# Kernel optimization log

Measured on AMD Instinct MI355X. Metric: run time of the kernel, lower is better.

Reference implementation:

```python
import jax, jax.numpy as jnp
import numpy as np

E, H, K = 8, 256, 2        # num_experts, hidden_size, top-k
B, S, TD, ID = 16, 1024, 768, 1024
EPS = 1e-5

def gelu(x):
    return jax.nn.gelu(x, approximate=False)  # torch nn.GELU default = exact erf

def layer_norm(x, g, b):
    m = jnp.mean(x, axis=-1, keepdims=True)
    v = jnp.var(x, axis=-1, keepdims=True)
    return (x - m) * jax.lax.rsqrt(v + EPS) * g + b

def moe(x, gate_W, gate_b, W1, b1, W2, b2):
    # x: [B,S,H]
    gates = jax.nn.softmax(x @ gate_W + gate_b, axis=-1)        # [B,S,E]
    topv, topi = jax.lax.top_k(gates, K)                        # [B,S,K]
    # dense all-expert compute (faithful to the torch loop+stack)
    h = gelu(jnp.einsum('bsh,ehg->bseg', x, W1) + b1)           # [B,S,E,H]
    eo = jnp.einsum('bseg,egh->bseh', h, W2) + b2               # [B,S,E,H]
    sel = jnp.take_along_axis(eo, topi[..., None], axis=2)      # [B,S,K,H]
    return jnp.sum(sel * topv[..., None], axis=2)               # [B,S,H]

def setup_inputs() -> dict:
    key = jax.random.key(0)
    ks = jax.random.split(key, 12)
    def n(k, shape, scale=0.05):
        return jax.random.normal(k, shape, jnp.float32) * scale
    return dict(
        x=jax.random.normal(ks[0], (B, S, TD), jnp.float32),
        We=n(ks[1], (TD, H)), be=jnp.zeros((H,), jnp.float32),
        l2_emb=n(ks[2], (H,)), cl_emb=n(ks[3], (H,)),
        gate_W=n(ks[4], (H, E)), gate_b=jnp.zeros((E,), jnp.float32),
        W1=n(ks[5], (E, H, H)), b1=jnp.zeros((E, H), jnp.float32),
        W2=n(ks[6], (E, H, H)), b2=jnp.zeros((E, H), jnp.float32),
        l2_g=jnp.ones((H,), jnp.float32), l2_b=jnp.zeros((H,), jnp.float32),
        cl_g=jnp.ones((H,), jnp.float32), cl_b=jnp.zeros((H,), jnp.float32),
        Wt2i=n(ks[7], (H, ID)), bt2i=jnp.zeros((ID,), jnp.float32),
        Wcl=n(ks[8], (H, H)), bcl=jnp.zeros((H,), jnp.float32),
    )

def reference(x, We, be, l2_emb, cl_emb, gate_W, gate_b, W1, b1, W2, b2,
              l2_g, l2_b, cl_g, cl_b, Wt2i, bt2i, Wcl, bcl):
    # task == 'text2image'
    x = gelu(x @ We + be)                                       # text_embed + gelu
    l2_in = x + l2_emb
    cl_in = x + cl_emb
    l2 = gelu(layer_norm(moe(l2_in, gate_W, gate_b, W1, b1, W2, b2), l2_g, l2_b)) + l2_in
    cl = gelu(layer_norm(moe(cl_in, gate_W, gate_b, W1, b1, W2, b2), cl_g, cl_b)) + cl_in
    l2_res = l2 @ Wt2i + bt2i                                   # text_to_image head
    cl_res = cl @ Wcl + bcl                                     # cl_text_to_image head
    return (l2_res, cl_res)
```

## Files before the change

### kernel.cpp

```cpp
#include <hip/hip_runtime.h>
#include <hip/hip_bf16.h>
#include <math.h>

typedef __bf16 bf16_t;
typedef __bf16 bf16x4 __attribute__((ext_vector_type(4)));
typedef __bf16 bf16x8 __attribute__((ext_vector_type(8)));
typedef float  f32x4  __attribute__((ext_vector_type(4)));

#define NTOK 16384
#define HD   256
#define TD   768
#define ID   1024
#define NPAIR 32768
#define MOE_TPB 520
#define FLAG_CAP 4096

__device__ inline float fast_erf(float x){
    float ax = fabsf(x);
    float t = 1.0f / (1.0f + 0.3275911f*ax);
    float y = t*(0.254829592f + t*(-0.284496736f + t*(1.421413741f +
              t*(-1.453152027f + t*1.061405429f))));
    float e = 1.0f - y*__expf(-ax*ax);
    return copysignf(e, x);
}
__device__ inline float gelu_f(float x){
    return 0.5f * x * (1.0f + fast_erf(x * 0.70710678118654752f));
}
__device__ inline bf16x4 cvt4(float4 a){
    bf16x4 o; o[0]=(bf16_t)a.x; o[1]=(bf16_t)a.y; o[2]=(bf16_t)a.z; o[3]=(bf16_t)a.w; return o;
}
__device__ inline f32x4 mfma16(bf16x8 a, bf16x8 b, f32x4 c){
    return __builtin_amdgcn_mfma_f32_16x16x32_bf16(a, b, c, 0, 0, 0);
}
__device__ inline void gload_lds16(const void* g, void* l){
    __builtin_amdgcn_global_load_lds(
        (const __attribute__((address_space(1))) unsigned int*)g,
        (__attribute__((address_space(3))) unsigned int*)l, 16, 0, 0);
}

__global__ void k_zero(int* meta){
    if (threadIdx.x < 64) meta[threadIdx.x] = 0;
}

__global__ __launch_bounds__(256) void k_convert(
    const float* __restrict__ We, const float* __restrict__ W1,
    const float* __restrict__ W2, const float* __restrict__ Wt,
    const float* __restrict__ Wc,
    bf16_t* __restrict__ WeHi, bf16_t* __restrict__ WeLo,
    bf16_t* __restrict__ W1T,
    bf16_t* __restrict__ W2T, bf16_t* __restrict__ WtT, bf16_t* __restrict__ WcT)
{
    __shared__ float T[64][65];
    int job = blockIdx.x;
    const float* src; bf16_t* dst; bf16_t* dst2 = nullptr;
    int K, N, k0, n0;
    if (job < 48){ src = We;  dst = WeHi; dst2 = WeLo; K = 768; N = 256;
        k0 = (job>>2)*64; n0 = (job&3)*64;
    } else if (job < 176){ int e = (job-48)>>4, tj = (job-48)&15;
        src = W1 + ((size_t)e<<16); dst = W1T + ((size_t)e<<16); K=256; N=256;
        k0 = (tj>>2)*64; n0 = (tj&3)*64;
    } else if (job < 304){ int e = (job-176)>>4, tj = (job-176)&15;
        src = W2 + ((size_t)e<<16); dst = W2T + ((size_t)e<<16); K=256; N=256;
        k0 = (tj>>2)*64; n0 = (tj&3)*64;
    } else if (job < 368){ int tj = job-304; src = Wt; dst = WtT; K=256; N=1024;
        k0 = (tj>>4)*64; n0 = (tj&15)*64;
    } else { int tj = job-368; src = Wc; dst = WcT; K=256; N=256;
        k0 = (tj>>2)*64; n0 = (tj&3)*64;
    }
    int t = threadIdx.x;
    #pragma unroll
    for (int u=0;u<4;++u){
        int unit = u*256 + t;
        int r = unit>>4, c4 = (unit&15)*4;
        float4 v = *(const float4*)(src + (size_t)(k0+r)*N + n0 + c4);
        T[r][c4] = v.x; T[r][c4+1] = v.y; T[r][c4+2] = v.z; T[r][c4+3] = v.w;
    }
    __syncthreads();
    #pragma unroll
    for (int u=0;u<4;++u){
        int unit = u*256 + t;
        int rn = unit>>4, c4 = (unit&15)*4;
        bf16x4 h, l;
        #pragma unroll
        for (int j=0;j<4;++j){
            float f = T[c4+j][rn];
            bf16_t hb = (bf16_t)f;
            h[j] = hb; l[j] = (bf16_t)(f - (float)hb);
        }
        *(bf16x4*)(dst + (size_t)(n0+rn)*K + k0 + c4) = h;
        if (dst2) *(bf16x4*)(dst2 + (size_t)(n0+rn)*K + k0 + c4) = l;
    }
}

__global__ __launch_bounds__(256) void k_embed(
    const float* __restrict__ x, const bf16_t* __restrict__ WeHi,
    const bf16_t* __restrict__ WeLo,
    const float* __restrict__ be, const float* __restrict__ l2e,
    const float* __restrict__ cle,
    float* __restrict__ l2f, float* __restrict__ clf)
{
    __shared__ bf16_t Ah[128][40];
    __shared__ bf16_t Al[128][40];
    __shared__ bf16_t Bh[64][40];
    __shared__ bf16_t Bl[64][40];
    int row0 = blockIdx.x*128, col0 = blockIdx.y*64;
    int t = threadIdx.x, wave = t>>6, lane = t&63;
    int wm = wave>>1, wn = wave&1;
    f32x4 acc[4][2] = {};
    for (int k0 = 0; k0 < TD; k0 += 32){
        __syncthreads();
        #pragma unroll
        for (int u=0; u<4; ++u){
            int fi = u*256 + t, r = fi>>3, q = fi&7;
            float4 v = *(const float4*)(x + (size_t)(row0+r)*TD + k0 + q*4);
            bf16x4 h = cvt4(v);
            float4 rl;
            rl.x = v.x-(float)h[0]; rl.y = v.y-(float)h[1];
            rl.z = v.z-(float)h[2]; rl.w = v.w-(float)h[3];
            *(bf16x4*)(&Ah[r][q*4]) = h;
            *(bf16x4*)(&Al[r][q*4]) = cvt4(rl);
        }
        {
            int r = t>>2, q = t&3;
            *(bf16x8*)(&Bh[r][q*8]) = *(const bf16x8*)(WeHi + (size_t)(col0+r)*TD + k0 + q*8);
            *(bf16x8*)(&Bl[r][q*8]) = *(const bf16x8*)(WeLo + (size_t)(col0+r)*TD + k0 + q*8);
        }
        __syncthreads();
        int kq = lane>>4, lr = lane&15;
        bf16x8 ah[4], al[4], bh[2], bl[2];
        #pragma unroll
        for (int m=0;m<4;++m){
            ah[m] = *(const bf16x8*)(&Ah[wm*64 + m*16 + lr][kq*8]);
            al[m] = *(const bf16x8*)(&Al[wm*64 + m*16 + lr][kq*8]);
        }
        #pragma unroll
        for (int n=0;n<2;++n){
            bh[n] = *(const bf16x8*)(&Bh[wn*32 + n*16 + lr][kq*8]);
            bl[n] = *(const bf16x8*)(&Bl[wn*32 + n*16 + lr][kq*8]);
        }
        #pragma unroll
        for (int m=0;m<4;++m)
            #pragma unroll
            for (int n=0;n<2;++n){
                acc[m][n] = mfma16(ah[m], bh[n], acc[m][n]);
                acc[m][n] = mfma16(ah[m], bl[n], acc[m][n]);
                acc[m][n] = mfma16(al[m], bh[n], acc[m][n]);
            }
    }
    int kq = lane>>4, lr = lane&15;
    #pragma unroll
    for (int n=0;n<2;++n){
        int col = col0 + wn*32 + n*16 + lr;
        float bv = be[col], lv = l2e[col], cv = cle[col];
        #pragma unroll
        for (int m=0;m<4;++m)
            #pragma unroll
            for (int r=0;r<4;++r){
                int row = row0 + wm*64 + m*16 + kq*4 + r;
                float v = gelu_f(acc[m][n][r] + bv);
                l2f[(size_t)row*HD + col] = v + lv;
                clf[(size_t)row*HD + col] = v + cv;
            }
    }
}

__global__ __launch_bounds__(256) void k_gate(
    const float* __restrict__ l2f, const float* __restrict__ clf,
    const float* __restrict__ gW, const float* __restrict__ gb,
    float* __restrict__ topv, int* __restrict__ topi,
    int* __restrict__ flaglist, int* __restrict__ nflag,
    bf16_t* __restrict__ l2h, bf16_t* __restrict__ clh)
{
    __shared__ float gw[2048];
    int t = threadIdx.x;
    for (int i=t; i<2048; i+=256) gw[i] = gW[i];
    __syncthreads();
    int wave = t>>6, lane = t&63;
    int idx = blockIdx.x*4 + wave;
    int br = idx>>14, tok = idx&16383;
    const float* in = br ? clf : l2f;
    float4 v = *(const float4*)(in + (size_t)tok*HD + lane*4);
    float xv[4] = {v.x, v.y, v.z, v.w};
    {
        bf16x4 hv; hv[0]=(bf16_t)v.x; hv[1]=(bf16_t)v.y; hv[2]=(bf16_t)v.z; hv[3]=(bf16_t)v.w;
        bf16_t* hout = br ? clh : l2h;
        *(bf16x4*)(hout + (size_t)tok*HD + lane*4) = hv;
    }
    float p[8];
    #pragma unroll
    for (int e=0;e<8;++e) p[e] = 0.f;
    #pragma unroll
    for (int j=0;j<4;++j){
        const float* g = &gw[(lane*4+j)*8];
        #pragma unroll
        for (int e=0;e<8;++e) p[e] += xv[j]*g[e];
    }
    #pragma unroll
    for (int e=0;e<8;++e){
        float s = p[e];
        #pragma unroll
        for (int o=32;o>0;o>>=1) s += __shfl_xor(s, o);
        p[e] = s + gb[e];
    }
    float mx = p[0];
    #pragma unroll
    for (int e=1;e<8;++e) mx = fmaxf(mx, p[e]);
    float den = 0.f;
    #pragma unroll
    for (int e=0;e<8;++e) den += expf(p[e]-mx);
    int i1 = 0; float m1 = p[0];
    #pragma unroll
    for (int e=1;e<8;++e) if (p[e] > m1){ m1 = p[e]; i1 = e; }
    int i2 = (i1==0)?1:0; float m2 = p[i2];
    #pragma unroll
    for (int e=0;e<8;++e) if (e != i1 && p[e] > m2){ m2 = p[e]; i2 = e; }
    if (lane == 0){
        topv[idx*2]   = expf(m1-mx)/den;
        topv[idx*2+1] = expf(m2-mx)/den;
        topi[idx*2]   = i1;
        topi[idx*2+1] = i2;
        float m3 = -1e30f;
        #pragma unroll
        for (int e=0;e<8;++e) if (e != i1 && e != i2) m3 = fmaxf(m3, p[e]);
        if (m2 - m3 < 1e-3f){
            int slot = atomicAdd(nflag, 1);
            if (slot < FLAG_CAP) flaglist[slot] = idx;
        }
    }
}

__global__ __launch_bounds__(256) void k_refine(
    const float* __restrict__ x, const float* __restrict__ We,
    const float* __restrict__ be,
    const float* __restrict__ l2e, const float* __restrict__ cle,
    const float* __restrict__ gW, const float* __restrict__ gb,
    const int* __restrict__ flaglist, const int* __restrict__ nflag,
    float* __restrict__ topv, int* __restrict__ topi)
{
    __shared__ float xs[768];
    __shared__ double red[256][8];
    int t = threadIdx.x;
    int nf = *nflag; if (nf > FLAG_CAP) nf = FLAG_CAP;
    for (int f = blockIdx.x; f < nf; f += gridDim.x){
        int idx = flaglist[f];
        int br = idx>>14, tok = idx&16383;
        __syncthreads();
        for (int i=t; i<768; i+=256) xs[i] = x[(size_t)tok*768 + i];
        __syncthreads();
        double u = 0.0;
        for (int j=0;j<768;++j) u += (double)xs[j] * (double)We[(size_t)j*256 + t];
        u += (double)be[t];
        double act = 0.5*u*(1.0 + erf(u*0.70710678118654752440));
        double li = act + (double)(br ? cle[t] : l2e[t]);
        #pragma unroll
        for (int e=0;e<8;++e) red[t][e] = li * (double)gW[t*8+e];
        __syncthreads();
        for (int s=128; s>0; s>>=1){
            if (t < s){
                #pragma unroll
                for (int e=0;e<8;++e) red[t][e] += red[t+s][e];
            }
            __syncthreads();
        }
        if (t == 0){
            double p[8];
            #pragma unroll
            for (int e=0;e<8;++e) p[e] = red[0][e] + (double)gb[e];
            int i1 = 0; double m1 = p[0];
            #pragma unroll
            for (int e=1;e<8;++e) if (p[e] > m1){ m1 = p[e]; i1 = e; }
            int i2 = (i1==0)?1:0; double m2 = p[i2];
            #pragma unroll
            for (int e=0;e<8;++e) if (e != i1 && p[e] > m2){ m2 = p[e]; i2 = e; }
            double mx = m1, den = 0.0;
            #pragma unroll
            for (int e=0;e<8;++e) den += exp(p[e]-mx);
            topv[idx*2]   = (float)(exp(m1-mx)/den);
            topv[idx*2+1] = (float)(exp(m2-mx)/den);
            topi[idx*2]   = i1;
            topi[idx*2+1] = i2;
        }
    }
}

__global__ __launch_bounds__(256) void k_hist(
    const int* __restrict__ topi, int* __restrict__ blockhist)
{
    __shared__ int h[16];
    int t = threadIdx.x;
    if (t < 16) h[t] = 0;
    __syncthreads();
    int idx = blockIdx.x*256 + t;
    int br = idx>>14;
    atomicAdd(&h[br*8 + topi[idx*2]], 1);
    atomicAdd(&h[br*8 + topi[idx*2+1]], 1);
    __syncthreads();
    if (t < 16) blockhist[blockIdx.x*16 + t] = h[t];
}

__global__ void k_scan(const int* __restrict__ blockhist, int* __restrict__ base,
                       int4* __restrict__ table)
{
    __shared__ int tot[16], off[16], tpre[2][9];
    int t = threadIdx.x;
    if (t < 16){
        int s = 0;
        for (int b=0;b<128;++b){ base[b*16+t] = s; s += blockhist[b*16+t]; }
        tot[t] = s;
    }
    __syncthreads();
    if (t == 0){
        for (int br=0;br<2;++br){
            int s=0, tp=0; tpre[br][0]=0;
            for (int e=0;e<8;++e){
                off[br*8+e]=s; s += tot[br*8+e];
                tp += (tot[br*8+e]+63)>>6; tpre[br][e+1]=tp;
            }
        }
    }
    __syncthreads();
    for (int i=t; i<2048; i+=256) base[i] += off[i&15];
    for (int i=t; i<2*MOE_TPB; i+=256){
        int b = i/MOE_TPB, ti = i%MOE_TPB;
        int4 ent = make_int4(-1,0,0,0);
        if (ti < tpre[b][8]){
            int e = 0;
            while (ti >= tpre[b][e+1]) ++e;
            int k = ti - tpre[b][e];
            int s = off[b*8+e] + k*64;
            int en = off[b*8+e] + tot[b*8+e];
            ent = make_int4(e, s, (s+64 < en) ? (s+64) : en, b);
        }
        table[i] = ent;
    }
}

__global__ __launch_bounds__(256) void k_scatter(
    const int* __restrict__ topi, const int* __restrict__ base,
    int* __restrict__ rows, int* __restrict__ posof)
{
    __shared__ int h[16];
    int t = threadIdx.x;
    if (t < 16) h[t] = 0;
    __syncthreads();
    int idx = blockIdx.x*256 + t;
    int br = idx>>14, tok = idx&16383;
    int e0 = topi[idx*2], e1 = topi[idx*2+1];
    int r0 = atomicAdd(&h[br*8+e0], 1);
    int r1 = atomicAdd(&h[br*8+e1], 1);
    int p0 = base[blockIdx.x*16 + br*8 + e0] + r0;
    int p1 = base[blockIdx.x*16 + br*8 + e1] + r1;
    rows[br*NPAIR + p0] = tok;
    rows[br*NPAIR + p1] = tok;
    posof[idx*2]   = p0;
    posof[idx*2+1] = p1;
}

__global__ __launch_bounds__(512, 4) void k_moe(
    const int4* __restrict__ table, const int* __restrict__ rows,
    const bf16_t* __restrict__ l2h, const bf16_t* __restrict__ clh,
    const bf16_t* __restrict__ W1T, const bf16_t* __restrict__ W2T,
    const float* __restrict__ b1, const float* __restrict__ b2,
    bf16_t* __restrict__ eo)
{
    int4 te = table[blockIdx.x];
    int e = te.x, start = te.y, end = te.z, br = te.w;
    if (e < 0) return;
    const bf16_t* inb = br ? clh : l2h;

    __shared__ bf16_t Ab[64*256];
    __shared__ bf16_t Bb[256*64];
    char* ab = (char*)Ab;
    char* bb = (char*)Bb;

    int t = threadIdx.x, w = t>>6, lane = t&63;
    int wm = w>>2, wn = w&3;
    int kq = lane>>4, lr = lane&15;

    #pragma unroll
    for (int u=0; u<4; ++u){
        int unit = (w*4+u)*64 + lane;
        int row = unit>>5, ch = unit&31;
        int pos = start + row;
        int tok = rows[br*NPAIR + ((pos < end) ? pos : start)];
        gload_lds16(inb + (size_t)tok*HD + ((ch ^ (row&7))<<3), ab + (w*4+u)*1024);
    }
    const bf16_t* W1e = W1T + ((size_t)e<<16);
    const bf16_t* W2e = W2T + ((size_t)e<<16);
    #pragma unroll
    for (int u=0; u<4; ++u){
        int unit = (w*4+u)*64 + lane;
        int row = unit>>3, c = unit&7;
        gload_lds16(W1e + (size_t)row*HD + ((c ^ (row&7))<<3), bb + (w*4+u)*1024);
    }
    __syncthreads();

    f32x4 acc[2][4] = {};
    for (int s=0; s<4; ++s){
        #pragma unroll
        for (int kk=0; kk<2; ++kk){
            bf16x8 af[2], bfr[4];
            #pragma unroll
            for (int m=0;m<2;++m){
                int row = wm*32 + m*16 + lr;
                int ch = s*8 + kk*4 + kq;
                af[m] = *(const bf16x8*)(ab + row*512 + ((ch ^ (row&7))<<4));
            }
            #pragma unroll
            for (int n=0;n<4;++n){
                int nc = wn*64 + n*16 + lr;
                int c = kk*4 + kq;
                bfr[n] = *(const bf16x8*)(bb + nc*128 + ((c ^ (nc&7))<<4));
            }
            #pragma unroll
            for (int m=0;m<2;++m)
                #pragma unroll
                for (int n=0;n<4;++n) acc[m][n] = mfma16(af[m], bfr[n], acc[m][n]);
        }
        __syncthreads();
        if (s < 3){
            #pragma unroll
            for (int u=0; u<4; ++u){
                int unit = (w*4+u)*64 + lane;
                int row = unit>>3, c = unit&7;
                gload_lds16(W1e + (size_t)row*HD + (s+1)*64 + ((c ^ (row&7))<<3),
                            bb + (w*4+u)*1024);
            }
            __syncthreads();
        }
    }
    #pragma unroll
    for (int u=0; u<4; ++u){
        int unit = (w*4+u)*64 + lane;
        int row = unit>>3, c = unit&7;
        gload_lds16(W2e + (size_t)row*HD + ((c ^ (row&7))<<3), bb + (w*4+u)*1024);
    }
    #pragma unroll
    for (int n=0;n<4;++n){
        int col = wn*64 + n*16 + lr;
        float bv = b1[e*256 + col];
        #pragma unroll
        for (int m=0;m<2;++m)
            #pragma unroll
            for (int r=0;r<4;++r){
                int row = wm*32 + m*16 + kq*4 + r;
                int byte = row*512 + ((((col>>3) ^ (row&7))<<4)) + (col&7)*2;
                *(bf16_t*)(ab + byte) = (bf16_t)gelu_f(acc[m][n][r] + bv);
            }
    }
    __syncthreads();
    #pragma unroll
    for (int m=0;m<2;++m)
        #pragma unroll
        for (int n=0;n<4;++n)
            #pragma unroll
            for (int r=0;r<4;++r) acc[m][n][r] = 0.f;
    for (int s=0; s<4; ++s){
        #pragma unroll
        for (int kk=0; kk<2; ++kk){
            bf16x8 af[2], bfr[4];
            #pragma unroll
            for (int m=0;m<2;++m){
                int row = wm*32 + m*16 + lr;
                int ch = s*8 + kk*4 + kq;
                af[m] = *(const bf16x8*)(ab + row*512 + ((ch ^ (row&7))<<4));
            }
            #pragma unroll
            for (int n=0;n<4;++n){
                int nc = wn*64 + n*16 + lr;
                int c = kk*4 + kq;
                bfr[n] = *(const bf16x8*)(bb + nc*128 + ((c ^ (nc&7))<<4));
            }
            #pragma unroll
            for (int m=0;m<2;++m)
                #pragma unroll
                for (int n=0;n<4;++n) acc[m][n] = mfma16(af[m], bfr[n], acc[m][n]);
        }
        if (s < 3){
            __syncthreads();
            #pragma unroll
            for (int u=0; u<4; ++u){
                int unit = (w*4+u)*64 + lane;
                int row = unit>>3, c = unit&7;
                gload_lds16(W2e + (size_t)row*HD + (s+1)*64 + ((c ^ (row&7))<<3),
                            bb + (w*4+u)*1024);
            }
            __syncthreads();
        }
    }
    #pragma unroll
    for (int n=0;n<4;++n){
        int col = wn*64 + n*16 + lr;
        float bv = b2[e*256 + col];
        #pragma unroll
        for (int m=0;m<2;++m)
            #pragma unroll
            for (int r=0;r<4;++r){
                int pos = start + wm*32 + m*16 + kq*4 + r;
                if (pos < end)
                    eo[((size_t)br*NPAIR + pos)*HD + col] = (bf16_t)(acc[m][n][r] + bv);
            }
    }
}

__global__ __launch_bounds__(256) void k_combine(
    const bf16_t* __restrict__ eo, const float* __restrict__ topv,
    const int* __restrict__ posof,
    const float* __restrict__ l2f, const float* __restrict__ clf,
    const float* __restrict__ l2g, const float* __restrict__ l2b,
    const float* __restrict__ clg, const float* __restrict__ clb,
    bf16_t* __restrict__ yl2, bf16_t* __restrict__ ycl)
{
    int t = threadIdx.x, wave = t>>6, lane = t&63;
    int idx = blockIdx.x*4 + wave;
    int br = idx>>14, tok = idx&16383;
    const float* in = br ? clf : l2f;
    const float* g  = br ? clg : l2g;
    const float* bb = br ? clb : l2b;
    bf16_t* y = br ? ycl : yl2;
    int p0 = posof[idx*2], p1 = posof[idx*2+1];
    float w0 = topv[idx*2], w1 = topv[idx*2+1];
    bf16x4 e0 = *(const bf16x4*)(eo + ((size_t)br*NPAIR + p0)*HD + lane*4);
    bf16x4 e1 = *(const bf16x4*)(eo + ((size_t)br*NPAIR + p1)*HD + lane*4);
    float v[4], s = 0.f, s2 = 0.f;
    #pragma unroll
    for (int j=0;j<4;++j){
        v[j] = w0*(float)e0[j] + w1*(float)e1[j];
        s += v[j]; s2 += v[j]*v[j];
    }
    #pragma unroll
    for (int o=32;o>0;o>>=1){ s += __shfl_xor(s, o); s2 += __shfl_xor(s2, o); }
    float mean = s * (1.f/256.f);
    float var  = s2 * (1.f/256.f) - mean*mean;
    float inv  = rsqrtf(var + 1e-5f);
    float4 iv = *(const float4*)(in + (size_t)tok*HD + lane*4);
    float ivv[4] = {iv.x, iv.y, iv.z, iv.w};
    bf16x4 ov;
    #pragma unroll
    for (int j=0;j<4;++j){
        int c = lane*4 + j;
        float ln = (v[j]-mean)*inv*g[c] + bb[c];
        ov[j] = (bf16_t)(gelu_f(ln) + ivv[j]);
    }
    *(bf16x4*)(y + (size_t)tok*HD + lane*4) = ov;
}

__global__ __launch_bounds__(256) void k_head(
    const bf16_t* __restrict__ A, const bf16_t* __restrict__ BT,
    const float* __restrict__ bias, float* __restrict__ out, int Nout)
{
    __shared__ bf16_t As[128][40];
    __shared__ bf16_t Bs[64][40];
    int row0 = blockIdx.x*128, col0 = blockIdx.y*64;
    int t = threadIdx.x, wave = t>>6, lane = t&63;
    int wm = wave>>1, wn = wave&1;
    f32x4 acc[4][2] = {};
    for (int k0=0; k0<HD; k0+=32){
        __syncthreads();
        #pragma unroll
        for (int u=0;u<2;++u){
            int fi = u*256 + t, r = fi>>2, q = fi&3;
            *(bf16x8*)(&As[r][q*8]) = *(const bf16x8*)(A + (size_t)(row0+r)*HD + k0 + q*8);
        }
        {
            int r = t>>2, q = t&3;
            *(bf16x8*)(&Bs[r][q*8]) = *(const bf16x8*)(BT + (size_t)(col0+r)*HD + k0 + q*8);
        }
        __syncthreads();
        int kq = lane>>4, lr = lane&15;
        bf16x8 af[4], bfr[2];
        #pragma unroll
        for (int m=0;m<4;++m) af[m] = *(const bf16x8*)(&As[wm*64 + m*16 + lr][kq*8]);
        #pragma unroll
        for (int n=0;n<2;++n) bfr[n] = *(const bf16x8*)(&Bs[wn*32 + n*16 + lr][kq*8]);
        #pragma unroll
        for (int m=0;m<4;++m)
            #pragma unroll
            for (int n=0;n<2;++n) acc[m][n] = mfma16(af[m], bfr[n], acc[m][n]);
    }
    int kq = lane>>4, lr = lane&15;
    #pragma unroll
    for (int n=0;n<2;++n){
        int col = col0 + wn*32 + n*16 + lr;
        float bv = bias[col];
        #pragma unroll
        for (int m=0;m<4;++m)
            #pragma unroll
            for (int r=0;r<4;++r){
                int row = row0 + wm*64 + m*16 + kq*4 + r;
                out[(size_t)row*Nout + col] = acc[m][n][r] + bv;
            }
    }
}

extern "C" void kernel_launch(void* const* d_in, const int* in_sizes, int n_in,
                              void* d_out, int out_size, void* d_ws, size_t ws_size,
                              hipStream_t stream)
{
    const float* x   = (const float*)d_in[0];
    const float* We  = (const float*)d_in[1];
    const float* be  = (const float*)d_in[2];
    const float* l2e = (const float*)d_in[3];
    const float* cle = (const float*)d_in[4];
    const float* gW  = (const float*)d_in[5];
    const float* gb  = (const float*)d_in[6];
    const float* W1  = (const float*)d_in[7];
    const float* b1  = (const float*)d_in[8];
    const float* W2  = (const float*)d_in[9];
    const float* b2  = (const float*)d_in[10];
    const float* l2g = (const float*)d_in[11];
    const float* l2b = (const float*)d_in[12];
    const float* clg = (const float*)d_in[13];
    const float* clb = (const float*)d_in[14];
    const float* Wt  = (const float*)d_in[15];
    const float* bt  = (const float*)d_in[16];
    const float* Wcl = (const float*)d_in[17];
    const float* bcl = (const float*)d_in[18];
    float* out = (float*)d_out;
    char* ws = (char*)d_ws;

    const size_t O_META  = 0;
    const size_t O_TABLE = 256;
    const size_t O_TOPV  = 17152;
    const size_t O_TOPI  = 279296;
    const size_t O_POSOF = 541440;
    const size_t O_ROWS  = 803584;
    const size_t O_WEHI  = 1065728;
    const size_t O_W1T   = 1458944;
    const size_t O_W2T   = 2507520;
    const size_t O_WTT   = 3556096;
    const size_t O_WCLT  = 4080384;
    const size_t O_L2F   = 4211456;
    const size_t O_CLF   = 20988672;
    const size_t O_EO    = 37765888;
    const size_t O_L2H   = 71320320;
    const size_t O_CLH   = 79708928;
    const size_t O_WELO  = 88097536;
    const size_t O_FLAG  = 88490752;
    const size_t O_BASE  = 88507136;
    const size_t O_BH    = 88515328;
    const size_t NEED    = 88523520;
    if (ws_size < NEED) return;

    int*    meta    = (int*)(ws + O_META);
    int*    nflag   = meta + 48;
    int4*   table   = (int4*)(ws + O_TABLE);
    int*    blockhist = (int*)(ws + O_BH);
    float*  topv    = (float*)(ws + O_TOPV);
    int*    topi    = (int*)(ws + O_TOPI);
    int*    posof   = (int*)(ws + O_POSOF);
    int*    rows    = (int*)(ws + O_ROWS);
    bf16_t* WeHi    = (bf16_t*)(ws + O_WEHI);
    bf16_t* WeLo    = (bf16_t*)(ws + O_WELO);
    int*    flaglist= (int*)(ws + O_FLAG);
    int*    basep   = (int*)(ws + O_BASE);
    bf16_t* W1T     = (bf16_t*)(ws + O_W1T);
    bf16_t* W2T     = (bf16_t*)(ws + O_W2T);
    bf16_t* WtT     = (bf16_t*)(ws + O_WTT);
    bf16_t* WcT     = (bf16_t*)(ws + O_WCLT);
    float*  l2f     = (float*)(ws + O_L2F);
    float*  clf     = (float*)(ws + O_CLF);
    bf16_t* eo      = (bf16_t*)(ws + O_EO);
    bf16_t* l2h     = (bf16_t*)(ws + O_L2H);
    bf16_t* clh     = (bf16_t*)(ws + O_CLH);
    bf16_t* yl2     = (bf16_t*)(ws + O_L2H);
    bf16_t* ycl     = (bf16_t*)(ws + O_CLH);

    k_zero<<<1, 64, 0, stream>>>(meta);
    k_convert<<<384, 256, 0, stream>>>(We, W1, W2, Wt, Wcl, WeHi, WeLo, W1T, W2T, WtT, WcT);
    k_embed<<<dim3(128,4), 256, 0, stream>>>(x, WeHi, WeLo, be, l2e, cle, l2f, clf);
    k_gate<<<8192, 256, 0, stream>>>(l2f, clf, gW, gb, topv, topi, flaglist, nflag, l2h, clh);
    k_refine<<<256, 256, 0, stream>>>(x, We, be, l2e, cle, gW, gb, flaglist, nflag, topv, topi);
    k_hist<<<128, 256, 0, stream>>>(topi, blockhist);
    k_scan<<<1, 256, 0, stream>>>(blockhist, basep, table);
    k_scatter<<<128, 256, 0, stream>>>(topi, basep, rows, posof);
    k_moe<<<2*MOE_TPB, 512, 0, stream>>>(table, rows, l2h, clh, W1T, W2T, b1, b2, eo);
    k_combine<<<8192, 256, 0, stream>>>(eo, topv, posof, l2f, clf, l2g, l2b, clg, clb, yl2, ycl);
    k_head<<<dim3(128,16), 256, 0, stream>>>(yl2, WtT, bt, out, 1024);
    k_head<<<dim3(128,4), 256, 0, stream>>>(ycl, WcT, bcl, out + (size_t)16777216, 256);
}
```

Baseline: 217.2 us.

## Pre-split x to bf16 hi/lo and double-buffer embed/head GEMMs via direct LDS loads

The fp32-to-bf16 hi/lo split of x moves into the convert kernel, which writes xh/xl into the expert-output workspace region before that region is reused. The embed and head GEMMs now use 512-thread blocks with double-buffered LDS filled by global_load_lds and an XOR-swizzled layout, so the next k-slice loads while MFMAs run. The per-wave tile shrinks and occupancy hints are added. In exchange, x makes an extra round trip through global memory and the convert grid grows to thousands of blocks.

Measured after the change: 226.1 us. 4.1% more time.

```diff
diff --git a/kernel.cpp b/kernel.cpp
--- a/kernel.cpp
+++ b/kernel.cpp
@@ -14,6 +14,7 @@
 #define NPAIR 32768
 #define MOE_TPB 520
 #define FLAG_CAP 4096
+#define XELEM 12582912
 
 __device__ inline float fast_erf(float x){
     float ax = fabsf(x);
@@ -43,15 +44,34 @@
 }
 
 __global__ __launch_bounds__(256) void k_convert(
+    const float* __restrict__ x,
     const float* __restrict__ We, const float* __restrict__ W1,
     const float* __restrict__ W2, const float* __restrict__ Wt,
     const float* __restrict__ Wc,
+    bf16_t* __restrict__ xh, bf16_t* __restrict__ xl,
     bf16_t* __restrict__ WeHi, bf16_t* __restrict__ WeLo,
     bf16_t* __restrict__ W1T,
     bf16_t* __restrict__ W2T, bf16_t* __restrict__ WtT, bf16_t* __restrict__ WcT)
 {
     __shared__ float T[64][65];
     int job = blockIdx.x;
+    int t = threadIdx.x;
+    if (job >= 384){
+        int i = (job-384)*2048 + t*8;
+        if (i < XELEM){
+            float4 v0 = *(const float4*)(x + i);
+            float4 v1 = *(const float4*)(x + i + 4);
+            bf16x4 h0 = cvt4(v0), h1 = cvt4(v1);
+            float4 r0, r1;
+            r0.x=v0.x-(float)h0[0]; r0.y=v0.y-(float)h0[1]; r0.z=v0.z-(float)h0[2]; r0.w=v0.w-(float)h0[3];
+            r1.x=v1.x-(float)h1[0]; r1.y=v1.y-(float)h1[1]; r1.z=v1.z-(float)h1[2]; r1.w=v1.w-(float)h1[3];
+            *(bf16x4*)(xh + i)     = h0;
+            *(bf16x4*)(xh + i + 4) = h1;
+            *(bf16x4*)(xl + i)     = cvt4(r0);
+            *(bf16x4*)(xl + i + 4) = cvt4(r1);
+        }
+        return;
+    }
     const float* src; bf16_t* dst; bf16_t* dst2 = nullptr;
     int K, N, k0, n0;
     if (job < 48){ src = We;  dst = WeHi; dst2 = WeLo; K = 768; N = 256;
@@ -67,7 +87,6 @@
     } else { int tj = job-368; src = Wc; dst = WcT; K=256; N=256;
         k0 = (tj>>2)*64; n0 = (tj&3)*64;
     }
-    int t = threadIdx.x;
     #pragma unroll
     for (int u=0;u<4;++u){
         int unit = u*256 + t;
@@ -92,71 +111,78 @@
     }
 }
 
-__global__ __launch_bounds__(256) void k_embed(
-    const float* __restrict__ x, const bf16_t* __restrict__ WeHi,
-    const bf16_t* __restrict__ WeLo,
+__global__ __launch_bounds__(512, 4) void k_embed(
+    const bf16_t* __restrict__ xh, const bf16_t* __restrict__ xl,
+    const bf16_t* __restrict__ WeHi, const bf16_t* __restrict__ WeLo,
     const float* __restrict__ be, const float* __restrict__ l2e,
     const float* __restrict__ cle,
     float* __restrict__ l2f, float* __restrict__ clf)
 {
-    __shared__ bf16_t Ah[128][40];
-    __shared__ bf16_t Al[128][40];
-    __shared__ bf16_t Bh[64][40];
-    __shared__ bf16_t Bl[64][40];
+    __shared__ bf16_t AhB[2][4096];
+    __shared__ bf16_t AlB[2][4096];
+    __shared__ bf16_t BhB[2][2048];
+    __shared__ bf16_t BlB[2][2048];
     int row0 = blockIdx.x*128, col0 = blockIdx.y*64;
-    int t = threadIdx.x, wave = t>>6, lane = t&63;
-    int wm = wave>>1, wn = wave&1;
-    f32x4 acc[4][2] = {};
-    for (int k0 = 0; k0 < TD; k0 += 32){
-        __syncthreads();
-        #pragma unroll
-        for (int u=0; u<4; ++u){
-            int fi = u*256 + t, r = fi>>3, q = fi&7;
-            float4 v = *(const float4*)(x + (size_t)(row0+r)*TD + k0 + q*4);
-            bf16x4 h = cvt4(v);
-            float4 rl;
-            rl.x = v.x-(float)h[0]; rl.y = v.y-(float)h[1];
-            rl.z = v.z-(float)h[2]; rl.w = v.w-(float)h[3];
-            *(bf16x4*)(&Ah[r][q*4]) = h;
-            *(bf16x4*)(&Al[r][q*4]) = cvt4(rl);
-        }
-        {
-            int r = t>>2, q = t&3;
-            *(bf16x8*)(&Bh[r][q*8]) = *(const bf16x8*)(WeHi + (size_t)(col0+r)*TD + k0 + q*8);
-            *(bf16x8*)(&Bl[r][q*8]) = *(const bf16x8*)(WeLo + (size_t)(col0+r)*TD + k0 + q*8);
-        }
-        __syncthreads();
-        int kq = lane>>4, lr = lane&15;
-        bf16x8 ah[4], al[4], bh[2], bl[2];
-        #pragma unroll
-        for (int m=0;m<4;++m){
-            ah[m] = *(const bf16x8*)(&Ah[wm*64 + m*16 + lr][kq*8]);
-            al[m] = *(const bf16x8*)(&Al[wm*64 + m*16 + lr][kq*8]);
+    int t = threadIdx.x, w = t>>6, lane = t&63;
+    int wm = w>>1, wn = w&1;
+    int kq = lane>>4, lr = lane&15;
+
+    auto stage = [&](int s, int p){
+        int rowA = t>>2, chA = t&3;
+        const size_t offA = (size_t)(row0+rowA)*TD + s*32 + ((chA ^ (rowA&3))<<3);
+        gload_lds16(xh + offA, (char*)AhB[p] + t*16);
+        gload_lds16(xl + offA, (char*)AlB[p] + t*16);
+        if (t < 256){
+            int rowB = t>>2, chB = t&3;
+            gload_lds16(WeHi + (size_t)(col0+rowB)*TD + s*32 + ((chB ^ (rowB&3))<<3),
+                        (char*)BhB[p] + t*16);
+        } else {
+            int tt = t-256, rowB = tt>>2, chB = tt&3;
+            gload_lds16(WeLo + (size_t)(col0+rowB)*TD + s*32 + ((chB ^ (rowB&3))<<3),
+                        (char*)BlB[p] + tt*16);
+        }
+    };
+
+    f32x4 acc[2][2] = {};
+    stage(0, 0);
+    __syncthreads();
+    for (int s=0; s<24; ++s){
+        int p = s&1;
+        if (s < 23) stage(s+1, p^1);
+        bf16x8 ah[2], al[2], bh[2], bl[2];
+        #pragma unroll
+        for (int m=0;m<2;++m){
+            int row = wm*32 + m*16 + lr;
+            int off = row*64 + ((kq ^ (row&3))<<4);
+            ah[m] = *(const bf16x8*)((char*)AhB[p] + off);
+            al[m] = *(const bf16x8*)((char*)AlB[p] + off);
         }
         #pragma unroll
         for (int n=0;n<2;++n){
-            bh[n] = *(const bf16x8*)(&Bh[wn*32 + n*16 + lr][kq*8]);
-            bl[n] = *(const bf16x8*)(&Bl[wn*32 + n*16 + lr][kq*8]);
-        }
-        #pragma unroll
-        for (int m=0;m<4;++m)
+            int nc = wn*32 + n*16 + lr;
+            int off = nc*64 + ((kq ^ (nc&3))<<4);
+            bh[n] = *(const bf16x8*)((char*)BhB[p] + off);
+            bl[n] = *(const bf16x8*)((char*)BlB[p] + off);
+        }
+        #pragma unroll
+        for (int m=0;m<2;++m)
             #pragma unroll
             for (int n=0;n<2;++n){
                 acc[m][n] = mfma16(ah[m], bh[n], acc[m][n]);
                 acc[m][n] = mfma16(ah[m], bl[n], acc[m][n]);
                 acc[m][n] = mfma16(al[m], bh[n], acc[m][n]);
             }
-    }
-    int kq = lane>>4, lr = lane&15;
+        __syncthreads();
+    }
     #pragma unroll
     for (int n=0;n<2;++n){
         int col = col0 + wn*32 + n*16 + lr;
         float bv = be[col], lv = l2e[col], cv = cle[col];
         #pragma unroll
-        for (int m=0;m<4;++m)
+        for (int m=0;m<2;++m)
             #pragma unroll
             for (int r=0;r<4;++r){
-                int row = row0 + wm*64 + m*16 + kq*4 + r;
+                int row = row0 + wm*32 + m*16 + kq*4 + r;
                 float v = gelu_f(acc[m][n][r] + bv);
                 l2f[(size_t)row*HD + col] = v + lv;
                 clf[(size_t)row*HD + col] = v + cv;
@@ -545,49 +571,66 @@
     *(bf16x4*)(y + (size_t)tok*HD + lane*4) = ov;
 }
 
-__global__ __launch_bounds__(256) void k_head(
+__global__ __launch_bounds__(512, 4) void k_head(
     const bf16_t* __restrict__ A, const bf16_t* __restrict__ BT,
     const float* __restrict__ bias, float* __restrict__ out, int Nout)
 {
-    __shared__ bf16_t As[128][40];
-    __shared__ bf16_t Bs[64][40];
+    __shared__ bf16_t AB[2][8192];
+    __shared__ bf16_t BB[2][4096];
     int row0 = blockIdx.x*128, col0 = blockIdx.y*64;
-    int t = threadIdx.x, wave = t>>6, lane = t&63;
-    int wm = wave>>1, wn = wave&1;
-    f32x4 acc[4][2] = {};
-    for (int k0=0; k0<HD; k0+=32){
+    int t = threadIdx.x, w = t>>6, lane = t&63;
+    int wm = w>>1, wn = w&1;
+    int kq = lane>>4, lr = lane&15;
+
+    auto stage = [&](int s, int p){
+        #pragma unroll
+        for (int u=0; u<2; ++u){
+            int unit = u*512 + t;
+            int rowA = unit>>3, chA = unit&7;
+            gload_lds16(A + (size_t)(row0+rowA)*HD + s*64 + ((chA ^ (rowA&7))<<3),
+                        (char*)AB[p] + unit*16);
+        }
+        int rowB = t>>3, chB = t&7;
+        gload_lds16(BT + (size_t)(col0+rowB)*HD + s*64 + ((chB ^ (rowB&7))<<3),
+                    (char*)BB[p] + t*16);
+    };
+
+    f32x4 acc[2][2] = {};
+    stage(0, 0);
+    __syncthreads();
+    for (int s=0; s<4; ++s){
+        int p = s&1;
+        if (s < 3) stage(s+1, p^1);
+        #pragma unroll
+        for (int kk=0; kk<2; ++kk){
+            int chunk = kk*4 + kq;
+            bf16x8 af[2], bfr[2];
+            #pragma unroll
+            for (int m=0;m<2;++m){
+                int row = wm*32 + m*16 + lr;
+                af[m] = *(const bf16x8*)((char*)AB[p] + row*128 + ((chunk ^ (row&7))<<4));
+            }
+            #pragma unroll
+            for (int n=0;n<2;++n){
+                int nc = wn*32 + n*16 + lr;
+                bfr[n] = *(const bf16x8*)((char*)BB[p] + nc*128 + ((chunk ^ (nc&7))<<4));
+            }
+            #pragma unroll
+            for (int m=0;m<2;++m)
+                #pragma unroll
+                for (int n=0;n<2;++n) acc[m][n] = mfma16(af[m], bfr[n], acc[m][n]);
+        }
         __syncthreads();
-        #pragma unroll
-        for (int u=0;u<2;++u){
-            int fi = u*256 + t, r = fi>>2, q = fi&3;
-            *(bf16x8*)(&As[r][q*8]) = *(const bf16x8*)(A + (size_t)(row0+r)*HD + k0 + q*8);
-        }
-        {
-            int r = t>>2, q = t&3;
-            *(bf16x8*)(&Bs[r][q*8]) = *(const bf16x8*)(BT + (size_t)(col0+r)*HD + k0 + q*8);
-        }
-        __syncthreads();
-        int kq = lane>>4, lr = lane&15;
-        bf16x8 af[4], bfr[2];
-        #pragma unroll
-        for (int m=0;m<4;++m) af[m] = *(const bf16x8*)(&As[wm*64 + m*16 + lr][kq*8]);
-        #pragma unroll
-        for (int n=0;n<2;++n) bfr[n] = *(const bf16x8*)(&Bs[wn*32 + n*16 + lr][kq*8]);
-        #pragma unroll
-        for (int m=0;m<4;++m)
-            #pragma unroll
-            for (int n=0;n<2;++n) acc[m][n] = mfma16(af[m], bfr[n], acc[m][n]);
-    }
-    int kq = lane>>4, lr = lane&15;
+    }
     #pragma unroll
     for (int n=0;n<2;++n){
         int col = col0 + wn*32 + n*16 + lr;
         float bv = bias[col];
         #pragma unroll
-        for (int m=0;m<4;++m)
+        for (int m=0;m<2;++m)
             #pragma unroll
             for (int r=0;r<4;++r){
-                int row = row0 + wm*64 + m*16 + kq*4 + r;
+                int row = row0 + wm*32 + m*16 + kq*4 + r;
                 out[(size_t)row*Nout + col] = acc[m][n][r] + bv;
             }
     }
@@ -661,14 +704,17 @@
     float*  l2f     = (float*)(ws + O_L2F);
     float*  clf     = (float*)(ws + O_CLF);
     bf16_t* eo      = (bf16_t*)(ws + O_EO);
+    bf16_t* xh      = (bf16_t*)(ws + O_EO);
+    bf16_t* xl      = xh + (size_t)XELEM;
     bf16_t* l2h     = (bf16_t*)(ws + O_L2H);
     bf16_t* clh     = (bf16_t*)(ws + O_CLH);
     bf16_t* yl2     = (bf16_t*)(ws + O_L2H);
     bf16_t* ycl     = (bf16_t*)(ws + O_CLH);
 
     k_zero<<<1, 64, 0, stream>>>(meta);
-    k_convert<<<384, 256, 0, stream>>>(We, W1, W2, Wt, Wcl, WeHi, WeLo, W1T, W2T, WtT, WcT);
-    k_embed<<<dim3(128,4), 256, 0, stream>>>(x, WeHi, WeLo, be, l2e, cle, l2f, clf);
+    k_convert<<<6528, 256, 0, stream>>>(x, We, W1, W2, Wt, Wcl, xh, xl,
+                                        WeHi, WeLo, W1T, W2T, WtT, WcT);
+    k_embed<<<dim3(128,4), 512, 0, stream>>>(xh, xl, WeHi, WeLo, be, l2e, cle, l2f, clf);
     k_gate<<<8192, 256, 0, stream>>>(l2f, clf, gW, gb, topv, topi, flaglist, nflag, l2h, clh);
     k_refine<<<256, 256, 0, stream>>>(x, We, be, l2e, cle, gW, gb, flaglist, nflag, topv, topi);
     k_hist<<<128, 256, 0, stream>>>(topi, blockhist);
@@ -676,6 +722,6 @@
     k_scatter<<<128, 256, 0, stream>>>(topi, basep, rows, posof);
     k_moe<<<2*MOE_TPB, 512, 0, stream>>>(table, rows, l2h, clh, W1T, W2T, b1, b2, eo);
     k_combine<<<8192, 256, 0, stream>>>(eo, topv, posof, l2f, clf, l2g, l2b, clg, clb, yl2, ycl);
-    k_head<<<dim3(128,16), 256, 0, stream>>>(yl2, WtT, bt, out, 1024);
-    k_head<<<dim3(128,4), 256, 0, stream>>>(ycl, WcT, bcl, out + (size_t)16777216, 256);
-}
+    k_head<<<dim3(128,16), 512, 0, stream>>>(yl2, WtT, bt, out, 1024);
+    k_head<<<dim3(128,4), 512, 0, stream>>>(ycl, WcT, bcl, out + (size_t)16777216, 256);
+}
```
